# Optimization experiments

Hardware: AMD Instinct MI355X
Metric: run time of the kernel (lower is better)

The kernel has to match this reference:

```python
import jax, jax.numpy as jnp
import numpy as np

NUM_HEADS = 16
ROPE_BASE = 50.0


def _apply_rope(x):
    # x: [b, s, h, d]; torchtune-style rotary embedding with base=ROPE_BASE
    b, s, h, d = x.shape
    inv_freq = 1.0 / (ROPE_BASE ** (jnp.arange(0, d, 2, dtype=jnp.float32) / d))  # [d/2]
    angles = jnp.arange(s, dtype=jnp.float32)[:, None] * inv_freq[None, :]         # [s, d/2]
    cos = jnp.cos(angles)[None, :, None, :]  # [1, s, 1, d/2]
    sin = jnp.sin(angles)[None, :, None, :]
    xr = x.reshape(b, s, h, d // 2, 2)
    x0, x1 = xr[..., 0], xr[..., 1]
    out = jnp.stack([x0 * cos - x1 * sin, x1 * cos + x0 * sin], axis=-1)
    return out.reshape(b, s, h, d).astype(x.dtype)


def setup_inputs() -> dict:
    key = jax.random.key(0)
    k1, k2, k3 = jax.random.split(key, 3)
    B, S, D = 2, 2048, 1024
    x = jax.random.normal(k1, (B, S, D), dtype=jnp.float32)
    w_qkv = jax.random.normal(k2, (3 * D, D), dtype=jnp.float32) * (D ** -0.5)
    w_out = jax.random.normal(k3, (D, D), dtype=jnp.float32) * (D ** -0.5)
    b_out = jnp.zeros((D,), dtype=jnp.float32)
    return {"x": x, "w_qkv": w_qkv, "w_out": w_out, "b_out": b_out}


def reference(x, w_qkv, w_out, b_out):
    B, S, D = x.shape
    H = NUM_HEADS
    dk = D // H

    qkv = x @ w_qkv.T                       # [b, s, 3D]
    q, k, v = jnp.split(qkv, 3, axis=-1)
    q = q.reshape(B, S, H, dk)
    k = k.reshape(B, S, H, dk)
    q = _apply_rope(q)
    k = _apply_rope(k)
    q = q.transpose(0, 2, 1, 3)             # [b, h, s, d]
    k = k.transpose(0, 2, 1, 3)
    v = v.reshape(B, S, H, dk).transpose(0, 2, 1, 3)

    scale = 1.0 / jnp.sqrt(jnp.asarray(dk, dtype=x.dtype))
    scores = jnp.einsum('bhsd,bhtd->bhst', q, k) * scale  # [b, h, s, s]
    # additive diagonal mask: -inf on the diagonal (blocks self-attention)
    eye = jnp.eye(S, dtype=bool)
    scores = jnp.where(eye[None, None], -jnp.inf, scores)
    attn = jax.nn.softmax(scores, axis=-1)
    out = jnp.einsum('bhst,bhtd->bhsd', attn, v)          # [b, h, s, d]
    out = out.transpose(0, 2, 1, 3).reshape(B, S, D)
    return out @ w_out.T + b_out
```

## Files before the change

### kernel.cpp

```cpp
#include <hip/hip_runtime.h>
#include <hip/hip_bf16.h>
#include <math.h>

#define D_MODEL 1024
#define NHEADS  16
#define DK      64
#define SEQ     2048
#define BATCH   2
#define QTILE   64

typedef __attribute__((ext_vector_type(8)))  short  short8;
typedef __attribute__((ext_vector_type(8)))  unsigned short ushort8;
typedef __attribute__((ext_vector_type(4)))  float  floatx4;
typedef __attribute__((ext_vector_type(16))) float  floatx16;

__device__ __forceinline__ unsigned short f2bf(float f) {
    union { float f; unsigned int u; } v; v.f = f;
    unsigned int u = v.u;
    return (unsigned short)((u + 0x7FFFu + ((u >> 16) & 1u)) >> 16);
}
__device__ __forceinline__ float bf2f(unsigned short u) {
    union { unsigned int u; float f; } v; v.u = ((unsigned int)u) << 16;
    return v.f;
}
__device__ __forceinline__ unsigned int fau(float f) {
    union { float f; unsigned int u; } v; v.f = f; return v.u;
}

__device__ __forceinline__ void gload_lds16(const unsigned short* g, unsigned short* l) {
    __builtin_amdgcn_global_load_lds((__attribute__((address_space(1))) const void*)g,
                                     (__attribute__((address_space(3))) void*)l,
                                     16, 0, 0);
}

#define X8 ((BATCH * SEQ * D_MODEL) / 8)
#define W8 ((3 * D_MODEL * D_MODEL) / 8)
#define O8 ((D_MODEL * D_MODEL) / 8)
__global__ __launch_bounds__(256) void pack_all(const float* __restrict__ x,
                                                const float* __restrict__ wq,
                                                const float* __restrict__ wo,
                                                unsigned short* __restrict__ xb,
                                                unsigned short* __restrict__ wqb,
                                                unsigned short* __restrict__ wob) {
    const int t = blockIdx.x * blockDim.x + threadIdx.x;
    const float* src; unsigned short* dst; int idx;
    if (t < X8)           { src = x;  dst = xb;  idx = t; }
    else if (t < X8 + W8) { src = wq; dst = wqb; idx = t - X8; }
    else if (t < X8 + W8 + O8) { src = wo; dst = wob; idx = t - X8 - W8; }
    else return;
    const float4 a = ((const float4*)src)[2 * idx];
    const float4 b = ((const float4*)src)[2 * idx + 1];
    short8 o;
    o[0] = (short)f2bf(a.x); o[1] = (short)f2bf(a.y);
    o[2] = (short)f2bf(a.z); o[3] = (short)f2bf(a.w);
    o[4] = (short)f2bf(b.x); o[5] = (short)f2bf(b.y);
    o[6] = (short)f2bf(b.z); o[7] = (short)f2bf(b.w);
    ((short8*)dst)[idx] = o;
}

template <int TM, typename OUT_T>
__global__ __launch_bounds__(256) void gemm_bf16(const unsigned short* __restrict__ A,
                                                 const unsigned short* __restrict__ B,
                                                 const float* __restrict__ bias,
                                                 OUT_T* __restrict__ C,
                                                 int M, int N, int K) {
    constexpr int NAF = TM / 32;
    __shared__ __align__(16) unsigned short As[TM][32];
    __shared__ __align__(16) unsigned short Bs[128][32];

    const int tid  = threadIdx.x;
    const int wave = tid >> 6;
    const int lane = tid & 63;
    const int quad = lane >> 4;
    const int lcol = lane & 15;
    const int wr   = (wave >> 1) * (TM / 2);
    const int wc   = (wave & 1) * 64;
    const int tm   = blockIdx.y * TM;
    const int tn   = blockIdx.x * 128;

    const int srowA = wave * (TM / 4) + (lane >> 2);
    const int srowB = wave * 32 + (lane >> 2);
    const int scol  = (lane & 3) * 8;
    const unsigned short* gB0 = B + (size_t)(tn + srowB) * K + scol;
    const unsigned short* gB1 = gB0 + (size_t)16 * K;
    unsigned short* lB0 = &Bs[wave * 32][0];
    unsigned short* lB1 = &Bs[wave * 32 + 16][0];

    floatx4 acc[NAF][4];
#pragma unroll
    for (int i = 0; i < NAF; ++i)
#pragma unroll
        for (int j = 0; j < 4; ++j) acc[i][j] = (floatx4){0.f, 0.f, 0.f, 0.f};

    for (int k0 = 0; k0 < K; k0 += 32) {
        __syncthreads();
#pragma unroll
        for (int u = 0; u < TM / 64; ++u)
            gload_lds16(A + (size_t)(tm + srowA + u * 16) * K + k0 + scol,
                        &As[wave * (TM / 4) + u * 16][0]);
        gload_lds16(gB0 + k0, lB0);
        gload_lds16(gB1 + k0, lB1);
        __syncthreads();

        short8 af[NAF], bf[4];
#pragma unroll
        for (int i = 0; i < NAF; ++i) af[i] = *(short8*)&As[wr + i * 16 + lcol][quad * 8];
#pragma unroll
        for (int j = 0; j < 4; ++j) bf[j] = *(short8*)&Bs[wc + j * 16 + lcol][quad * 8];
#pragma unroll
        for (int i = 0; i < NAF; ++i)
#pragma unroll
            for (int j = 0; j < 4; ++j)
                acc[i][j] = __builtin_amdgcn_mfma_f32_16x16x32_bf16(af[i], bf[j], acc[i][j], 0, 0, 0);
    }

#pragma unroll
    for (int i = 0; i < NAF; ++i) {
#pragma unroll
        for (int r = 0; r < 4; ++r) {
            const int row = tm + wr + i * 16 + quad * 4 + r;
#pragma unroll
            for (int j = 0; j < 4; ++j) {
                const int col = tn + wc + j * 16 + lcol;
                float v = acc[i][j][r];
                if (bias) v += bias[col];
                if constexpr (sizeof(OUT_T) == 2)
                    C[(size_t)row * N + col] = (OUT_T)f2bf(v);
                else
                    C[(size_t)row * N + col] = (OUT_T)v;
            }
        }
    }
}

__global__ __launch_bounds__(256) void rope_vtrans(const unsigned short* __restrict__ qkvb,
                                                   unsigned short* __restrict__ Qb,
                                                   unsigned short* __restrict__ Kb,
                                                   unsigned short* __restrict__ Vtg) {
    const int st = blockIdx.x, h = blockIdx.y, b = blockIdx.z;
    const int tid = threadIdx.x;
    const int s0 = st * 64;

    const int i  = tid & 31;
    const int r0 = tid >> 5;
    const float inv_freq = exp2f(-(2.0f * (float)i / (float)DK) * log2f(50.0f));
    const float QSCALE = 0.125f * 1.44269504f;
#pragma unroll
    for (int pass = 0; pass < 8; ++pass) {
        const int s = s0 + r0 + pass * 8;
        const size_t in_base = ((size_t)(b * SEQ + s)) * (3 * D_MODEL) + h * DK + 2 * i;
        const float q0 = bf2f(qkvb[in_base]),           q1 = bf2f(qkvb[in_base + 1]);
        const float k0 = bf2f(qkvb[in_base + D_MODEL]), k1 = bf2f(qkvb[in_base + D_MODEL + 1]);
        float sn, cs;
        __sincosf((float)s * inv_freq, &sn, &cs);
        const size_t ob = (((size_t)(b * NHEADS + h)) * SEQ + s) * DK + 2 * i;
        const unsigned int qw = (unsigned int)f2bf((q0 * cs - q1 * sn) * QSCALE)
                              | ((unsigned int)f2bf((q1 * cs + q0 * sn) * QSCALE) << 16);
        const unsigned int kw = (unsigned int)f2bf(k0 * cs - k1 * sn)
                              | ((unsigned int)f2bf(k1 * cs + k0 * sn) << 16);
        *(unsigned int*)&Qb[ob] = qw;
        *(unsigned int*)&Kb[ob] = kw;
    }

    __shared__ unsigned short Lt[64][65];
    const int r = tid >> 3;
    const int c = (tid & 7) * 8;
    const size_t in_row = ((size_t)(b * SEQ + s0 + r)) * (3 * D_MODEL) + 2 * D_MODEL + h * DK + c;
    const ushort8 v0 = *(const ushort8*)&qkvb[in_row];
    const ushort8 v1 = *(const ushort8*)&qkvb[in_row + (size_t)32 * (3 * D_MODEL)];
    const int u0 = r, u1 = r + 32;
    const int kc0 = (u0 & 48) | (8 * ((u0 >> 2) & 1) + (u0 & 3) + 4 * ((u0 >> 3) & 1));
    const int kc1 = (u1 & 48) | (8 * ((u1 >> 2) & 1) + (u1 & 3) + 4 * ((u1 >> 3) & 1));
#pragma unroll
    for (int j = 0; j < 8; ++j) Lt[c + j][kc0] = v0[j];
#pragma unroll
    for (int j = 0; j < 8; ++j) Lt[c + j][kc1] = v1[j];
    __syncthreads();
    const size_t bh = (size_t)(b * NHEADS + h);
    ushort8 o0, o1;
#pragma unroll
    for (int j = 0; j < 8; ++j) { o0[j] = Lt[r][c + j]; o1[j] = Lt[r + 32][c + j]; }
    unsigned short* orow = Vtg + (bh * DK + r) * SEQ + s0 + c;
    *(ushort8*)orow = o0;
    *(ushort8*)(orow + (size_t)32 * SEQ) = o1;
}

#define LDW 72

__global__ __launch_bounds__(256, 4) void flash_attn(const unsigned short* __restrict__ Qb,
                                                     const unsigned short* __restrict__ Kb,
                                                     const unsigned short* __restrict__ Vtg,
                                                     unsigned short* __restrict__ attnb) {
    const int qt   = blockIdx.x;
    const int h    = blockIdx.y;
    const int b    = blockIdx.z;
    const int tid  = threadIdx.x;
    const int wave = tid >> 6;
    const int lane = tid & 63;
    const int l31  = lane & 31;
    const int lh   = lane >> 5;
    const int mh   = wave & 1;
    const int kh   = wave >> 1;
    const int kb   = kh * 32;

    __shared__ __align__(16) unsigned char smem[2 * 64 * LDW * 2];
    unsigned short (*Ks)[LDW] = (unsigned short (*)[LDW])smem;
    unsigned short (*Vt)[LDW] = (unsigned short (*)[LDW])(smem + 64 * LDW * 2);
    float (*Ored)[68] = (float (*)[68])smem;
    float* lred0 = (float*)(smem + 64 * 68 * 4);
    float* lred1 = lred0 + 64;

    const size_t bh = (size_t)(b * NHEADS + h);
    const unsigned short* Qg = Qb + (bh * SEQ + (size_t)qt * QTILE) * DK;
    const unsigned short* Kg = Kb + bh * SEQ * DK;
    const unsigned short* Vg = Vtg + bh * (size_t)DK * SEQ;

    short8 qf[4];
#pragma unroll
    for (int t = 0; t < 4; ++t)
        qf[t] = *(const short8*)&Qg[(size_t)(mh * 32 + l31) * DK + t * 16 + lh * 8];

    const int strow = tid >> 3;
    const int stcol = (tid & 7) * 8;
    const unsigned short* kg0 = &Kg[(size_t)strow * DK + stcol];
    const unsigned short* kg1 = &Kg[(size_t)(strow + 32) * DK + stcol];
    const unsigned short* vg0 = &Vg[(size_t)strow * SEQ + stcol];
    const unsigned short* vg1 = &Vg[(size_t)(strow + 32) * SEQ + stcol];

    short8 kr0 = *(const short8*)&kg0[0];
    short8 kr1 = *(const short8*)&kg1[0];
    short8 vr0 = *(const short8*)&vg0[0];
    short8 vr1 = *(const short8*)&vg1[0];

    floatx16 oacc[2];
    oacc[0] = (floatx16)(0.f);
    oacc[1] = (floatx16)(0.f);
    float lp = 0.f;

    const int diag_kt = qt * QTILE;

    for (int kt = 0; kt < SEQ; kt += 64) {
        __syncthreads();
        *(short8*)&Ks[strow][stcol]      = kr0;
        *(short8*)&Ks[strow + 32][stcol] = kr1;
        *(short8*)&Vt[strow][stcol]      = vr0;
        *(short8*)&Vt[strow + 32][stcol] = vr1;
        __syncthreads();

        const int ktn = (kt + 64 < SEQ) ? kt + 64 : 0;
        kr0 = *(const short8*)&kg0[(size_t)ktn * DK];
        kr1 = *(const short8*)&kg1[(size_t)ktn * DK];
        vr0 = *(const short8*)&vg0[ktn];
        vr1 = *(const short8*)&vg1[ktn];

        floatx16 sc = (floatx16)(0.f);
#pragma unroll
        for (int t = 0; t < 4; ++t) {
            const short8 kf = *(short8*)&Ks[kb + l31][t * 16 + lh * 8];
            sc = __builtin_amdgcn_mfma_f32_32x32x16_bf16(kf, qf[t], sc, 0, 0, 0);
        }

        if (kt == diag_kt && kh == mh) {
#pragma unroll
            for (int r = 0; r < 16; ++r) {
                const int key_loc = (r & 3) + 8 * (r >> 2) + 4 * lh;
                if (key_loc == l31) sc[r] = -1e30f;
            }
        }

        short8 pf0, pf1;
        {
            union { unsigned int u[4]; short8 s8; } a, c;
#pragma unroll
            for (int d = 0; d < 4; ++d) {
                const float e0 = __builtin_amdgcn_exp2f(sc[2 * d]);
                const float e1 = __builtin_amdgcn_exp2f(sc[2 * d + 1]);
                a.u[d] = __builtin_amdgcn_perm(fau(e1), fau(e0), 0x07060302u);
                const float f0 = __builtin_amdgcn_exp2f(sc[8 + 2 * d]);
                const float f1 = __builtin_amdgcn_exp2f(sc[8 + 2 * d + 1]);
                c.u[d] = __builtin_amdgcn_perm(fau(f1), fau(f0), 0x07060302u);
                lp += (e0 + e1) + (f0 + f1);
            }
            pf0 = a.s8;
            pf1 = c.s8;
        }

#pragma unroll
        for (int nd = 0; nd < 2; ++nd) {
            const short8 vfa = *(short8*)&Vt[nd * 32 + l31][kb + lh * 8];
            const short8 vfb = *(short8*)&Vt[nd * 32 + l31][kb + 16 + lh * 8];
            oacc[nd] = __builtin_amdgcn_mfma_f32_32x32x16_bf16(pf0, vfa, oacc[nd], 0, 0, 0);
            oacc[nd] = __builtin_amdgcn_mfma_f32_32x32x16_bf16(pf1, vfb, oacc[nd], 0, 0, 0);
        }
    }

    const float lptot = lp + __shfl_xor(lp, 32, 64);

    __syncthreads();
    if (lh == 0) {
        if (kh == 0) lred0[mh * 32 + l31] = lptot;
        else         lred1[mh * 32 + l31] = lptot;
    }
    if (kh == 1) {
#pragma unroll
        for (int r = 0; r < 16; ++r) {
            const int m = mh * 32 + (r & 3) + 8 * (r >> 2) + 4 * lh;
            Ored[m][l31]      = oacc[0][r];
            Ored[m][32 + l31] = oacc[1][r];
        }
    }
    __syncthreads();
    if (kh == 0) {
        unsigned short* obase = attnb + ((size_t)b * SEQ + (size_t)qt * QTILE) * D_MODEL + h * DK;
#pragma unroll
        for (int r = 0; r < 16; ++r) {
            const int m = mh * 32 + (r & 3) + 8 * (r >> 2) + 4 * lh;
            const float inv = 1.001953125f / (lred0[m] + lred1[m]);
            const float v0 = (oacc[0][r] + Ored[m][l31]) * inv;
            const float v1 = (oacc[1][r] + Ored[m][32 + l31]) * inv;
            obase[(size_t)m * D_MODEL + l31]      = f2bf(v0);
            obase[(size_t)m * D_MODEL + 32 + l31] = f2bf(v1);
        }
    }
}

extern "C" void kernel_launch(void* const* d_in, const int* in_sizes, int n_in,
                              void* d_out, int out_size, void* d_ws, size_t ws_size,
                              hipStream_t stream) {
    const float* x     = (const float*)d_in[0];
    const float* w_qkv = (const float*)d_in[1];
    const float* w_out = (const float*)d_in[2];
    const float* b_out = (const float*)d_in[3];
    float* out = (float*)d_out;

    const int M = BATCH * SEQ;
    const size_t X_ELEMS    = (size_t)M * D_MODEL;
    const size_t WQKV_ELEMS = (size_t)3 * D_MODEL * D_MODEL;
    const size_t WOUT_ELEMS = (size_t)D_MODEL * D_MODEL;
    const size_t QKV_ELEMS  = (size_t)M * 3 * D_MODEL;
    const size_t HEAD_ELEMS = (size_t)BATCH * NHEADS * SEQ * DK;

    unsigned short* xb    = (unsigned short*)d_ws;
    unsigned short* wqkvb = xb + X_ELEMS;
    unsigned short* woutb = wqkvb + WQKV_ELEMS;
    unsigned short* qkvb  = woutb + WOUT_ELEMS;
    unsigned short* Qb    = qkvb + QKV_ELEMS;
    unsigned short* Kb    = Qb + HEAD_ELEMS;
    unsigned short* Vtg   = Kb + HEAD_ELEMS;
    unsigned short* attnb = Vtg + HEAD_ELEMS;

    pack_all<<<(X8 + W8 + O8 + 255) / 256, 256, 0, stream>>>(x, w_qkv, w_out, xb, wqkvb, woutb);

    {
        dim3 grid(3 * D_MODEL / 128, M / 128);
        gemm_bf16<128, unsigned short><<<grid, 256, 0, stream>>>(xb, wqkvb, nullptr, qkvb,
                                                                 M, 3 * D_MODEL, D_MODEL);
    }
    {
        dim3 grid(SEQ / 64, NHEADS, BATCH);
        rope_vtrans<<<grid, 256, 0, stream>>>(qkvb, Qb, Kb, Vtg);
    }
    {
        dim3 grid(SEQ / QTILE, NHEADS, BATCH);
        flash_attn<<<grid, 256, 0, stream>>>(Qb, Kb, Vtg, attnb);
    }
    {
        dim3 grid(D_MODEL / 128, M / 64);
        gemm_bf16<64, float><<<grid, 256, 0, stream>>>(attnb, woutb, b_out, out,
                                                       M, D_MODEL, D_MODEL);
    }
}
```

Before: 201.9 us.

## Double-buffer K/V tiles, widen Q tile to 128 with 8 waves, remap blocks

The attention kernel now handles 128 query rows per block with 8 waves, so each K/V tile loaded into shared memory feeds twice as many queries. K/V staging is double-buffered, which leaves one barrier per 64-key tile, and the mask diagonal check is computed per wave. It adds s_setprio around the MFMA sections and remaps the flat block id so neighbouring blocks spread across heads and batches. The block now uses more LDS and more threads, which may lower occupancy.

```diff
diff --git a/kernel.cpp b/kernel.cpp
--- a/kernel.cpp
+++ b/kernel.cpp
@@ -7,7 +7,7 @@
 #define DK      64
 #define SEQ     2048
 #define BATCH   2
-#define QTILE   64
+#define QTILE   128
 
 typedef __attribute__((ext_vector_type(8)))  short  short8;
 typedef __attribute__((ext_vector_type(8)))  unsigned short ushort8;
@@ -187,28 +187,33 @@
 
 #define LDW 72
 
-__global__ __launch_bounds__(256, 4) void flash_attn(const unsigned short* __restrict__ Qb,
+__global__ __launch_bounds__(512, 4) void flash_attn(const unsigned short* __restrict__ Qb,
                                                      const unsigned short* __restrict__ Kb,
                                                      const unsigned short* __restrict__ Vtg,
                                                      unsigned short* __restrict__ attnb) {
-    const int qt   = blockIdx.x;
-    const int h    = blockIdx.y;
-    const int b    = blockIdx.z;
     const int tid  = threadIdx.x;
     const int wave = tid >> 6;
     const int lane = tid & 63;
     const int l31  = lane & 31;
     const int lh   = lane >> 5;
-    const int mh   = wave & 1;
-    const int kh   = wave >> 1;
+    const int mh2  = wave & 3;
+    const int kh   = wave >> 2;
     const int kb   = kh * 32;
 
-    __shared__ __align__(16) unsigned char smem[2 * 64 * LDW * 2];
-    unsigned short (*Ks)[LDW] = (unsigned short (*)[LDW])smem;
-    unsigned short (*Vt)[LDW] = (unsigned short (*)[LDW])(smem + 64 * LDW * 2);
+    const int f  = blockIdx.x + gridDim.x * (blockIdx.y + gridDim.y * blockIdx.z);
+    const int w  = (f & 7) * 64 + (f >> 3);
+    const int qt = w & 15;
+    const int h  = (w >> 4) & 15;
+    const int b  = w >> 8;
+
+    __shared__ __align__(16) unsigned char smem[36864];
+    unsigned short (*Ks0)[LDW] = (unsigned short (*)[LDW])(smem);
+    unsigned short (*Vt0)[LDW] = (unsigned short (*)[LDW])(smem +  9216);
+    unsigned short (*Ks1)[LDW] = (unsigned short (*)[LDW])(smem + 18432);
+    unsigned short (*Vt1)[LDW] = (unsigned short (*)[LDW])(smem + 27648);
     float (*Ored)[68] = (float (*)[68])smem;
-    float* lred0 = (float*)(smem + 64 * 68 * 4);
-    float* lred1 = lred0 + 64;
+    float* lred0 = (float*)(smem + 34816);
+    float* lred1 = lred0 + 128;
 
     const size_t bh = (size_t)(b * NHEADS + h);
     const unsigned short* Qg = Qb + (bh * SEQ + (size_t)qt * QTILE) * DK;
@@ -218,49 +223,34 @@
     short8 qf[4];
 #pragma unroll
     for (int t = 0; t < 4; ++t)
-        qf[t] = *(const short8*)&Qg[(size_t)(mh * 32 + l31) * DK + t * 16 + lh * 8];
+        qf[t] = *(const short8*)&Qg[(size_t)(mh2 * 32 + l31) * DK + t * 16 + lh * 8];
 
     const int strow = tid >> 3;
     const int stcol = (tid & 7) * 8;
-    const unsigned short* kg0 = &Kg[(size_t)strow * DK + stcol];
-    const unsigned short* kg1 = &Kg[(size_t)(strow + 32) * DK + stcol];
-    const unsigned short* vg0 = &Vg[(size_t)strow * SEQ + stcol];
-    const unsigned short* vg1 = &Vg[(size_t)(strow + 32) * SEQ + stcol];
-
-    short8 kr0 = *(const short8*)&kg0[0];
-    short8 kr1 = *(const short8*)&kg1[0];
-    short8 vr0 = *(const short8*)&vg0[0];
-    short8 vr1 = *(const short8*)&vg1[0];
+    const unsigned short* kg = &Kg[(size_t)strow * DK + stcol];
+    const unsigned short* vg = &Vg[(size_t)strow * SEQ + stcol];
+
+    short8 kr = *(const short8*)&kg[0];
+    short8 vr = *(const short8*)&vg[0];
 
     floatx16 oacc[2];
     oacc[0] = (floatx16)(0.f);
     oacc[1] = (floatx16)(0.f);
     float lp = 0.f;
 
-    const int diag_kt = qt * QTILE;
-
-    for (int kt = 0; kt < SEQ; kt += 64) {
-        __syncthreads();
-        *(short8*)&Ks[strow][stcol]      = kr0;
-        *(short8*)&Ks[strow + 32][stcol] = kr1;
-        *(short8*)&Vt[strow][stcol]      = vr0;
-        *(short8*)&Vt[strow + 32][stcol] = vr1;
-        __syncthreads();
-
-        const int ktn = (kt + 64 < SEQ) ? kt + 64 : 0;
-        kr0 = *(const short8*)&kg0[(size_t)ktn * DK];
-        kr1 = *(const short8*)&kg1[(size_t)ktn * DK];
-        vr0 = *(const short8*)&vg0[ktn];
-        vr1 = *(const short8*)&vg1[ktn];
-
+    const int diagkt = qt * QTILE + mh2 * 32 - kb;
+
+    auto compute = [&](unsigned short (*Ks)[LDW], unsigned short (*Vt)[LDW], int kt) {
         floatx16 sc = (floatx16)(0.f);
+        __builtin_amdgcn_s_setprio(1);
 #pragma unroll
         for (int t = 0; t < 4; ++t) {
             const short8 kf = *(short8*)&Ks[kb + l31][t * 16 + lh * 8];
             sc = __builtin_amdgcn_mfma_f32_32x32x16_bf16(kf, qf[t], sc, 0, 0, 0);
         }
-
-        if (kt == diag_kt && kh == mh) {
+        __builtin_amdgcn_s_setprio(0);
+
+        if (kt == diagkt) {
 #pragma unroll
             for (int r = 0; r < 16; ++r) {
                 const int key_loc = (r & 3) + 8 * (r >> 2) + 4 * lh;
@@ -285,6 +275,7 @@
             pf1 = c.s8;
         }
 
+        __builtin_amdgcn_s_setprio(1);
 #pragma unroll
         for (int nd = 0; nd < 2; ++nd) {
             const short8 vfa = *(short8*)&Vt[nd * 32 + l31][kb + lh * 8];
@@ -292,19 +283,37 @@
             oacc[nd] = __builtin_amdgcn_mfma_f32_32x32x16_bf16(pf0, vfa, oacc[nd], 0, 0, 0);
             oacc[nd] = __builtin_amdgcn_mfma_f32_32x32x16_bf16(pf1, vfb, oacc[nd], 0, 0, 0);
         }
+        __builtin_amdgcn_s_setprio(0);
+    };
+
+    for (int kt = 0; kt < SEQ; kt += 128) {
+        *(short8*)&Ks0[strow][stcol] = kr;
+        *(short8*)&Vt0[strow][stcol] = vr;
+        __syncthreads();
+        kr = *(const short8*)&kg[(size_t)(kt + 64) * DK];
+        vr = *(const short8*)&vg[kt + 64];
+        compute(Ks0, Vt0, kt);
+
+        *(short8*)&Ks1[strow][stcol] = kr;
+        *(short8*)&Vt1[strow][stcol] = vr;
+        __syncthreads();
+        const int ktn = (kt + 128 < SEQ) ? kt + 128 : 0;
+        kr = *(const short8*)&kg[(size_t)ktn * DK];
+        vr = *(const short8*)&vg[ktn];
+        compute(Ks1, Vt1, kt + 64);
     }
 
     const float lptot = lp + __shfl_xor(lp, 32, 64);
 
     __syncthreads();
     if (lh == 0) {
-        if (kh == 0) lred0[mh * 32 + l31] = lptot;
-        else         lred1[mh * 32 + l31] = lptot;
+        if (kh == 0) lred0[mh2 * 32 + l31] = lptot;
+        else         lred1[mh2 * 32 + l31] = lptot;
     }
     if (kh == 1) {
 #pragma unroll
         for (int r = 0; r < 16; ++r) {
-            const int m = mh * 32 + (r & 3) + 8 * (r >> 2) + 4 * lh;
+            const int m = mh2 * 32 + (r & 3) + 8 * (r >> 2) + 4 * lh;
             Ored[m][l31]      = oacc[0][r];
             Ored[m][32 + l31] = oacc[1][r];
         }
@@ -314,7 +323,7 @@
         unsigned short* obase = attnb + ((size_t)b * SEQ + (size_t)qt * QTILE) * D_MODEL + h * DK;
 #pragma unroll
         for (int r = 0; r < 16; ++r) {
-            const int m = mh * 32 + (r & 3) + 8 * (r >> 2) + 4 * lh;
+            const int m = mh2 * 32 + (r & 3) + 8 * (r >> 2) + 4 * lh;
             const float inv = 1.001953125f / (lred0[m] + lred1[m]);
             const float v0 = (oacc[0][r] + Ored[m][l31]) * inv;
             const float v1 = (oacc[1][r] + Ored[m][32 + l31]) * inv;
@@ -362,7 +371,7 @@
     }
     {
         dim3 grid(SEQ / QTILE, NHEADS, BATCH);
-        flash_attn<<<grid, 256, 0, stream>>>(Qb, Kb, Vtg, attnb);
+        flash_attn<<<grid, 512, 0, stream>>>(Qb, Kb, Vtg, attnb);
     }
     {
         dim3 grid(D_MODEL / 128, M / 64);
```

Result: faster. 195.2 us (-3.3%).
